# Kernel optimization log

Hardware: AMD Instinct MI355X
Metric: run time of the kernel (lower is better)

The kernel has to match this reference:

```python
import jax, jax.numpy as jnp
import numpy as np

IN_CH = 256
OUT_CH = 256
K = 3
STRIDE = 1
PAD = 1
NUM_EMB = 8


def setup_inputs() -> dict:
    key = jax.random.key(0)
    ks = jax.random.split(key, 6)
    B, H, W = 16, 64, 64
    x = jax.random.normal(ks[0], (B, IN_CH, H, W), dtype=jnp.float32)
    kernal_embed = jax.random.normal(ks[1], (NUM_EMB, IN_CH, OUT_CH, K, K), dtype=jnp.float32)
    # 1x1 conv params (stored as a dense [out,in] matrix) + bias
    cls_conv_w = jax.random.normal(ks[2], (IN_CH, IN_CH), dtype=jnp.float32) / np.sqrt(IN_CH)
    cls_conv_b = jax.random.normal(ks[3], (IN_CH,), dtype=jnp.float32) * 0.01
    cls_dense_w = jax.random.normal(ks[4], (NUM_EMB, IN_CH), dtype=jnp.float32) / np.sqrt(IN_CH)
    cls_dense_b = jax.random.normal(ks[5], (NUM_EMB,), dtype=jnp.float32) * 0.01
    return {"x": x, "kernal_embed": kernal_embed, "cls_conv_w": cls_conv_w,
            "cls_conv_b": cls_conv_b, "cls_dense_w": cls_dense_w, "cls_dense_b": cls_dense_b}


def reference(x, kernal_embed, cls_conv_w, cls_conv_b, cls_dense_w, cls_dense_b):
    B, C, H, W = x.shape
    # 1x1 conv -> global avg pool -> dense -> softmax weights over embeddings
    w = jnp.einsum('bchw,dc->bdhw', x, cls_conv_w) + cls_conv_b[None, :, None, None]
    pooled = jnp.mean(w, axis=(2, 3))                       # (B, C)
    logits = pooled @ cls_dense_w.T + cls_dense_b           # (B, E)
    mix = jax.nn.softmax(logits, axis=1)                    # (B, E)
    # Per-sample kernel synthesis: (B, in, out, k, k)
    kern = jnp.einsum('be,eiojk->biojk', mix, kernal_embed)
    # Faithful to torch .view(-1, in, k, k): raw reshape (mixes in/out axes as in original)
    kern = kern.reshape(B, OUT_CH, IN_CH, K, K)
    # Grouped conv with groups=B == per-sample conv via vmap
    def conv1(xi, wi):
        # xi: (C, H, W), wi: (out, in, k, k)
        return jax.lax.conv_general_dilated(
            xi[None], wi, window_strides=(STRIDE, STRIDE),
            padding=[(PAD, PAD), (PAD, PAD)],
            dimension_numbers=('NCHW', 'OIHW', 'NCHW'))[0]
    out = jax.vmap(conv1)(x, kern)                          # (B, out, H, W)
    return out
```

## Files before the change

kernel.cpp:

```cpp
#include <hip/hip_runtime.h>
#include <stdint.h>

#define B_  16
#define C_  256
#define H_  64
#define W_  64
#define P_  4096
#define E_  8
#define HP_ 66

typedef __bf16 bf16x8 __attribute__((ext_vector_type(8)));
typedef float  f32x4  __attribute__((ext_vector_type(4)));

__device__ __forceinline__ unsigned short f2bf(float f) {
    union { float f; unsigned int u; } v; v.f = f;
    unsigned int u = v.u;
    unsigned int r = (u + 0x7fffu + ((u >> 16) & 1u)) >> 16;
    return (unsigned short)r;
}

__device__ __forceinline__ void async_load16(const void* g, void* l) {
    __builtin_amdgcn_global_load_lds(
        (const __attribute__((address_space(1))) void*)g,
        (__attribute__((address_space(3))) void*)l, 16, 0, 0);
}

__global__ void k_xpose(const float* __restrict__ x, unsigned short* __restrict__ Xp,
                        float* __restrict__ xsum) {
    const int bid = blockIdx.x;
    const int tid = threadIdx.x;

    if (bid < 520) {
        const int gid = bid * 256 + tid;
        const int pix = gid >> 5;
        const int chunk = gid & 31;
        const int bb = pix / 260;
        const int j = pix - bb * 260;
        int h, w;
        if (j < 66)       { h = 0;  w = j; }
        else if (j < 132) { h = 65; w = j - 66; }
        else { int jj = j - 132; h = 1 + (jj & 63); w = (jj < 64) ? 0 : 65; }
        const uint4 z = {0u, 0u, 0u, 0u};
        *(uint4*)(Xp + ((size_t)((bb * HP_ + h) * HP_ + w) << 8) + chunk * 8) = z;
    }

    const int b  = bid >> 8;
    const int h  = (bid >> 2) & 63;
    const int cg = bid & 3;
    const int c0 = cg << 6;
    __shared__ float tile[64][65];
    {
        const int ci = tid >> 2, wseg = tid & 3;
        const float* src = x + ((size_t)(b * 256 + c0 + ci) << 12) + (h << 6) + wseg * 16;
        float s = 0.f;
#pragma unroll
        for (int i = 0; i < 4; ++i) {
            float4 v = *(const float4*)(src + i * 4);
            tile[ci][wseg * 16 + i * 4 + 0] = v.x;
            tile[ci][wseg * 16 + i * 4 + 1] = v.y;
            tile[ci][wseg * 16 + i * 4 + 2] = v.z;
            tile[ci][wseg * 16 + i * 4 + 3] = v.w;
            s += v.x + v.y + v.z + v.w;
        }
        s += __shfl_down(s, 1, 64);
        s += __shfl_down(s, 2, 64);
        if ((tid & 3) == 0) atomicAdd(&xsum[b * 256 + c0 + ci], s);
    }
    __syncthreads();
    {
        const int w = tid >> 2, cs = tid & 3;
        unsigned short ov[16] __attribute__((aligned(16)));
#pragma unroll
        for (int k = 0; k < 16; ++k) ov[k] = f2bf(tile[cs * 16 + k][w]);
        unsigned short* dst = Xp + ((size_t)((b * HP_ + h + 1) * HP_ + (w + 1)) << 8) + c0 + cs * 16;
        ((uint4*)dst)[0] = ((const uint4*)ov)[0];
        ((uint4*)dst)[1] = ((const uint4*)ov)[1];
    }
}

__global__ void k_mix(const float* __restrict__ xsum,
                      const float* __restrict__ cw, const float* __restrict__ cb,
                      const float* __restrict__ dw, const float* __restrict__ db,
                      float* __restrict__ mix) {
    const int b = blockIdx.x, tid = threadIdx.x;
    __shared__ __align__(16) float sxm[256];
    __shared__ __align__(16) float spool[256];
    __shared__ float sl[8];
    sxm[tid] = xsum[b * 256 + tid] * (1.0f / P_);
    __syncthreads();
    {
        float a = cb[tid];
        const float4* cwr = (const float4*)(cw + (size_t)tid * 256);
        const float4* xv4 = (const float4*)sxm;
#pragma unroll 8
        for (int c = 0; c < 64; ++c) {
            const float4 wv = cwr[c];
            const float4 xv = xv4[c];
            a += wv.x * xv.x + wv.y * xv.y + wv.z * xv.z + wv.w * xv.w;
        }
        spool[tid] = a;
    }
    __syncthreads();
    if (tid < 64) {
        const int e = tid >> 3, dl = tid & 7;
        float part = 0.f;
#pragma unroll 4
        for (int d = dl; d < 256; d += 8) part += dw[e * 256 + d] * spool[d];
        part += __shfl_down(part, 4, 64);
        part += __shfl_down(part, 2, 64);
        part += __shfl_down(part, 1, 64);
        if (dl == 0) sl[e] = part + db[e];
    }
    __syncthreads();
    if (tid < 8) {
        float m = sl[0];
        for (int e = 1; e < 8; ++e) m = fmaxf(m, sl[e]);
        float den = 0.f;
        for (int e = 0; e < 8; ++e) den += __expf(sl[e] - m);
        mix[b * 8 + tid] = __expf(sl[tid] - m) / den;
    }
}

__global__ void k_mixkern(const float* __restrict__ KE, const float* __restrict__ mix,
                          unsigned short* __restrict__ Wg) {
    const int o    = blockIdx.x >> 1;
    const int half = blockIdx.x & 1;
    const int ic0  = half << 7;
    const int tid  = threadIdx.x;
    __shared__ __align__(16) float s[8][1152];
    __shared__ float smix[128];
    if (tid < 128) smix[tid] = mix[tid];
#pragma unroll
    for (int e = 0; e < 8; ++e) {
        const float4* src = (const float4*)(KE + (size_t)(e * 256 + o) * 2304 + ic0 * 9);
        float4* dst = (float4*)s[e];
        dst[tid] = src[tid];
        if (tid < 32) dst[256 + tid] = src[256 + tid];
    }
    __syncthreads();
    const int icl = tid & 127;
    const int b0  = (tid >> 7) << 3;
#pragma unroll
    for (int t = 0; t < 9; ++t) {
        float v[8];
#pragma unroll
        for (int e = 0; e < 8; ++e) v[e] = s[e][icl * 9 + t];
#pragma unroll
        for (int bb = 0; bb < 8; ++bb) {
            const int b = b0 + bb;
            float acc = 0.f;
#pragma unroll
            for (int e = 0; e < 8; ++e) acc += smix[b * 8 + e] * v[e];
            Wg[((size_t)(b * 256 + o) * 9 + t) * 256 + ic0 + icl] = f2bf(acc);
        }
    }
}

__global__ __launch_bounds__(256) void k_gemm(const unsigned short* __restrict__ Wg,
                                              const unsigned short* __restrict__ Xp,
                                              float* __restrict__ out) {
    __shared__ __align__(16) unsigned short lA[128 * 64];
    __shared__ __align__(16) unsigned short lB[128 * 64];
    const int tid = threadIdx.x;
    const int bid = blockIdx.x;
    const int xcd = bid & 7;
    const int g   = bid >> 3;
    const int b   = xcd + ((g >> 6) << 3);
    const int rem = g & 63;
    const int ot  = rem & 1;
    const int rp  = rem >> 1;
    const int o0  = ot << 7;
    const int h0  = rp << 1;

    const int wid  = tid >> 6;
    const int lane = tid & 63;
    const int wm   = wid >> 1;
    const int wn   = wid & 1;
    const int ql   = lane & 15;
    const int quad = lane >> 4;
    const int sw   = ql & 7;

    const int srow = tid >> 3;
    const int sseg = tid & 7;
    const int csrc = sseg ^ (srow & 7);

    f32x4 acc[4][4];
#pragma unroll
    for (int i = 0; i < 4; ++i)
#pragma unroll
        for (int j = 0; j < 4; ++j) acc[i][j] = (f32x4)0.0f;

    char* lAb = (char*)lA;
    char* lBb = (char*)lB;
    const size_t abase = (size_t)(b * 256 + o0 + srow) * 9 * 256 + csrc * 8;

    for (int t = 0; t < 9; ++t) {
        const int kh = t / 3;
        const int kw = t - kh * 3;
        for (int kc = 0; kc < 4; ++kc) {
#pragma unroll
            for (int j = 0; j < 4; ++j) {
                const unsigned short* ga = Wg + abase + (size_t)j * 32 * 9 * 256
                                           + (size_t)t * 256 + kc * 64;
                async_load16(ga, lAb + tid * 16 + j * 4096);
            }
#pragma unroll
            for (int j = 0; j < 4; ++j) {
                const int pix = srow + 32 * j;
                const int pr  = pix >> 6;
                const int w   = pix & 63;
                const unsigned short* gb = Xp
                    + ((size_t)((b * HP_ + h0 + pr + kh) * HP_ + (w + kw)) << 8)
                    + kc * 64 + csrc * 8;
                async_load16(gb, lBb + tid * 16 + j * 4096);
            }
            __syncthreads();
#pragma unroll
            for (int kk = 0; kk < 2; ++kk) {
                bf16x8 af[4], bv[4];
#pragma unroll
                for (int mi = 0; mi < 4; ++mi)
                    af[mi] = *(const bf16x8*)(lAb + (wm * 64 + mi * 16 + ql) * 128
                                              + ((((kk << 2) | quad) ^ sw) << 4));
#pragma unroll
                for (int ni = 0; ni < 4; ++ni)
                    bv[ni] = *(const bf16x8*)(lBb + (wn * 64 + ni * 16 + ql) * 128
                                              + ((((kk << 2) | quad) ^ sw) << 4));
#pragma unroll
                for (int mi = 0; mi < 4; ++mi)
#pragma unroll
                    for (int ni = 0; ni < 4; ++ni)
                        acc[mi][ni] = __builtin_amdgcn_mfma_f32_16x16x32_bf16(
                            af[mi], bv[ni], acc[mi][ni], 0, 0, 0);
            }
            __syncthreads();
        }
    }

    const int h = h0 + wn;
#pragma unroll
    for (int mi = 0; mi < 4; ++mi) {
        const int o = o0 + wm * 64 + mi * 16 + quad * 4;
#pragma unroll
        for (int ni = 0; ni < 4; ++ni) {
            const int w = ni * 16 + ql;
            float* po = out + ((size_t)(b * 256 + o) << 12) + (h << 6) + w;
#pragma unroll
            for (int r = 0; r < 4; ++r) po[(size_t)r << 12] = acc[mi][ni][r];
        }
    }
}

extern "C" void kernel_launch(void* const* d_in, const int* in_sizes, int n_in,
                              void* d_out, int out_size, void* d_ws, size_t ws_size,
                              hipStream_t stream) {
    const float* x  = (const float*)d_in[0];
    const float* KE = (const float*)d_in[1];
    const float* cw = (const float*)d_in[2];
    const float* cb = (const float*)d_in[3];
    const float* dw = (const float*)d_in[4];
    const float* db = (const float*)d_in[5];
    float* out = (float*)d_out;

    char* ws = (char*)d_ws;
    float* xsum           = (float*)(ws + 0);
    float* mix            = (float*)(ws + 16384);
    unsigned short* Wg    = (unsigned short*)(ws + 32768);
    unsigned short* Xp    = (unsigned short*)(ws + 32768 + 18874368);

    hipMemsetAsync(xsum, 0, B_ * C_ * sizeof(float), stream);
    k_xpose  <<<dim3(B_ * H_ * 4),    dim3(256), 0, stream>>>(x, Xp, xsum);
    k_mix    <<<dim3(B_),             dim3(256), 0, stream>>>(xsum, cw, cb, dw, db, mix);
    k_mixkern<<<dim3(C_ * 2),         dim3(256), 0, stream>>>(KE, mix, Wg);
    k_gemm   <<<dim3(B_ * 2 * 32),    dim3(256), 0, stream>>>(Wg, Xp, out);
}
```

Measured before the change: 259.0 us.

## Restructure conv GEMM into 256x256 tiles with double-buffered async pipeline

Rewrites the implicit-GEMM conv kernel to use 512-thread blocks computing all 256 output channels by 256 pixels (4 rows), with 8 waves each holding 8x4 MFMA accumulators. LDS is double-buffered for both A and B, and global_load_lds prefetches of the next K-stage are interleaved with MFMA phases using explicit s_barrier/s_waitcnt and s_setprio. The larger tile halves redundant reloads of the input and weight tiles, and the software pipeline hides load latency behind compute. In exchange, the grid shrinks to 256 blocks, register pressure rises, and correctness depends on hand-placed barriers and vmcnt counts.

After: 253.5 us. 2.1% less time.

```diff
diff --git a/kernel.cpp b/kernel.cpp
--- a/kernel.cpp
+++ b/kernel.cpp
@@ -156,97 +156,117 @@
     }
 }
 
-__global__ __launch_bounds__(256) void k_gemm(const unsigned short* __restrict__ Wg,
-                                              const unsigned short* __restrict__ Xp,
-                                              float* __restrict__ out) {
-    __shared__ __align__(16) unsigned short lA[128 * 64];
-    __shared__ __align__(16) unsigned short lB[128 * 64];
+__global__ __launch_bounds__(512, 2) void k_gemm(const unsigned short* __restrict__ Wg,
+                                                 const unsigned short* __restrict__ Xp,
+                                                 float* __restrict__ out) {
+    __shared__ __align__(16) unsigned short L[4][16384];
     const int tid = threadIdx.x;
     const int bid = blockIdx.x;
     const int xcd = bid & 7;
     const int g   = bid >> 3;
-    const int b   = xcd + ((g >> 6) << 3);
-    const int rem = g & 63;
-    const int ot  = rem & 1;
-    const int rp  = rem >> 1;
-    const int o0  = ot << 7;
-    const int h0  = rp << 1;
+    const int b   = xcd + ((g >> 4) << 3);
+    const int tile = g & 15;
+    const int h0  = tile << 2;
 
     const int wid  = tid >> 6;
     const int lane = tid & 63;
-    const int wm   = wid >> 1;
-    const int wn   = wid & 1;
+    const int wm   = wid >> 2;
+    const int wn   = wid & 3;
     const int ql   = lane & 15;
     const int quad = lane >> 4;
     const int sw   = ql & 7;
 
     const int srow = tid >> 3;
-    const int sseg = tid & 7;
-    const int csrc = sseg ^ (srow & 7);
-
-    f32x4 acc[4][4];
-#pragma unroll
-    for (int i = 0; i < 4; ++i)
+    const int csrc = (tid & 7) ^ (srow & 7);
+
+    f32x4 acc[8][4];
+#pragma unroll
+    for (int i = 0; i < 8; ++i)
 #pragma unroll
         for (int j = 0; j < 4; ++j) acc[i][j] = (f32x4)0.0f;
 
-    char* lAb = (char*)lA;
-    char* lBb = (char*)lB;
-    const size_t abase = (size_t)(b * 256 + o0 + srow) * 9 * 256 + csrc * 8;
-
-    for (int t = 0; t < 9; ++t) {
-        const int kh = t / 3;
-        const int kw = t - kh * 3;
-        for (int kc = 0; kc < 4; ++kc) {
-#pragma unroll
-            for (int j = 0; j < 4; ++j) {
-                const unsigned short* ga = Wg + abase + (size_t)j * 32 * 9 * 256
-                                           + (size_t)t * 256 + kc * 64;
-                async_load16(ga, lAb + tid * 16 + j * 4096);
-            }
-#pragma unroll
-            for (int j = 0; j < 4; ++j) {
-                const int pix = srow + 32 * j;
-                const int pr  = pix >> 6;
-                const int w   = pix & 63;
-                const unsigned short* gb = Xp
-                    + ((size_t)((b * HP_ + h0 + pr + kh) * HP_ + (w + kw)) << 8)
-                    + kc * 64 + csrc * 8;
-                async_load16(gb, lBb + tid * 16 + j * 4096);
-            }
-            __syncthreads();
-#pragma unroll
-            for (int kk = 0; kk < 2; ++kk) {
-                bf16x8 af[4], bv[4];
-#pragma unroll
-                for (int mi = 0; mi < 4; ++mi)
-                    af[mi] = *(const bf16x8*)(lAb + (wm * 64 + mi * 16 + ql) * 128
-                                              + ((((kk << 2) | quad) ^ sw) << 4));
-#pragma unroll
-                for (int ni = 0; ni < 4; ++ni)
-                    bv[ni] = *(const bf16x8*)(lBb + (wn * 64 + ni * 16 + ql) * 128
-                                              + ((((kk << 2) | quad) ^ sw) << 4));
-#pragma unroll
-                for (int mi = 0; mi < 4; ++mi)
-#pragma unroll
-                    for (int ni = 0; ni < 4; ++ni)
-                        acc[mi][ni] = __builtin_amdgcn_mfma_f32_16x16x32_bf16(
-                            af[mi], bv[ni], acc[mi][ni], 0, 0, 0);
-            }
-            __syncthreads();
-        }
-    }
-
-    const int h = h0 + wn;
-#pragma unroll
-    for (int mi = 0; mi < 4; ++mi) {
-        const int o = o0 + wm * 64 + mi * 16 + quad * 4;
-#pragma unroll
-        for (int ni = 0; ni < 4; ++ni) {
-            const int w = ni * 16 + ql;
-            float* po = out + ((size_t)(b * 256 + o) << 12) + (h << 6) + w;
-#pragma unroll
-            for (int r = 0; r < 4; ++r) po[(size_t)r << 12] = acc[mi][ni][r];
+    auto stageA = [&](int s, int P) {
+        const int t = s >> 2, kc = s & 3;
+        const unsigned short* ga = Wg + ((size_t)(b * 256 + srow) * 9 + t) * 256
+                                   + kc * 64 + csrc * 8;
+#pragma unroll
+        for (int j = 0; j < 4; ++j)
+            async_load16(ga + (size_t)j * 64 * 9 * 256, (char*)L[P] + tid * 16 + j * 8192);
+    };
+    auto stageB = [&](int s, int P) {
+        const int t = s >> 2, kc = s & 3;
+        const int kh = t / 3, kw = t - kh * 3;
+#pragma unroll
+        for (int j = 0; j < 4; ++j)
+            async_load16(Xp + (((size_t)((b * HP_ + h0 + j + kh) * HP_ + (srow + kw))) << 8)
+                             + kc * 64 + csrc * 8,
+                         (char*)L[2 + P] + tid * 16 + j * 8192);
+    };
+
+    bf16x8 af[4], bv[4];
+
+#define PH(AP, BP, KK, MH, READB, PREF_STMT, VM_STMT)                              \
+    do {                                                                           \
+        _Pragma("unroll")                                                          \
+        for (int r_ = 0; r_ < 4; ++r_)                                             \
+            af[r_] = *(const bf16x8*)((const char*)L[AP]                           \
+                     + (wm * 128 + ((MH) * 4 + r_) * 16 + ql) * 128                \
+                     + (((((KK) << 2) | quad) ^ sw) << 4));                        \
+        if (READB) {                                                               \
+            _Pragma("unroll")                                                      \
+            for (int r_ = 0; r_ < 4; ++r_)                                         \
+                bv[r_] = *(const bf16x8*)((const char*)L[BP]                       \
+                         + (wn * 64 + r_ * 16 + ql) * 128                          \
+                         + (((((KK) << 2) | quad) ^ sw) << 4));                    \
+        }                                                                          \
+        PREF_STMT;                                                                 \
+        asm volatile("s_barrier" ::: "memory");                                    \
+        asm volatile("s_waitcnt lgkmcnt(0)" ::: "memory");                         \
+        __builtin_amdgcn_s_setprio(1);                                             \
+        _Pragma("unroll")                                                          \
+        for (int r_ = 0; r_ < 4; ++r_)                                             \
+            _Pragma("unroll")                                                      \
+            for (int n_ = 0; n_ < 4; ++n_)                                         \
+                acc[(MH) * 4 + r_][n_] = __builtin_amdgcn_mfma_f32_16x16x32_bf16(  \
+                    af[r_], bv[n_], acc[(MH) * 4 + r_][n_], 0, 0, 0);              \
+        __builtin_amdgcn_s_setprio(0);                                             \
+        VM_STMT;                                                                   \
+        asm volatile("s_barrier" ::: "memory");                                    \
+    } while (0)
+
+    stageA(0, 0); stageB(0, 0); stageB(1, 1);
+    asm volatile("s_waitcnt vmcnt(4)" ::: "memory");
+    asm volatile("s_barrier" ::: "memory");
+
+    for (int i = 0; i < 18; ++i) {
+        const int sE = 2 * i;
+        const int sO = sE + 1;
+        const bool pf = (i < 17);
+        PH(0, 2, 0, 0, 1, stageA(sO, 1), ((void)0));
+        PH(0, 2, 0, 1, 0, ((void)0), ((void)0));
+        PH(0, 2, 1, 0, 1, ((void)0), ((void)0));
+        PH(0, 2, 1, 1, 0,
+           if (pf) stageB(sE + 2, 0),
+           if (pf) { asm volatile("s_waitcnt vmcnt(4)" ::: "memory"); }
+           else    { asm volatile("s_waitcnt vmcnt(0)" ::: "memory"); });
+        PH(1, 3, 0, 0, 1, if (pf) stageA(sE + 2, 0), ((void)0));
+        PH(1, 3, 0, 1, 0, ((void)0), ((void)0));
+        PH(1, 3, 1, 0, 1, ((void)0), ((void)0));
+        PH(1, 3, 1, 1, 0,
+           if (pf) stageB(sO + 2, 1),
+           if (pf) { asm volatile("s_waitcnt vmcnt(4)" ::: "memory"); });
+    }
+#undef PH
+
+#pragma unroll
+    for (int m = 0; m < 8; ++m) {
+        const int o = wm * 128 + m * 16 + quad * 4;
+#pragma unroll
+        for (int n = 0; n < 4; ++n) {
+            const int w = n * 16 + ql;
+            float* po = out + ((size_t)(b * 256 + o) << 12) + ((h0 + wn) << 6) + w;
+#pragma unroll
+            for (int r = 0; r < 4; ++r) po[(size_t)r << 12] = acc[m][n][r];
         }
     }
 }
@@ -272,5 +292,5 @@
     k_xpose  <<<dim3(B_ * H_ * 4),    dim3(256), 0, stream>>>(x, Xp, xsum);
     k_mix    <<<dim3(B_),             dim3(256), 0, stream>>>(xsum, cw, cb, dw, db, mix);
     k_mixkern<<<dim3(C_ * 2),         dim3(256), 0, stream>>>(KE, mix, Wg);
-    k_gemm   <<<dim3(B_ * 2 * 32),    dim3(256), 0, stream>>>(Wg, Xp, out);
-}
+    k_gemm   <<<dim3(256),            dim3(512), 0, stream>>>(Wg, Xp, out);
+}
```
